# Kernel optimization log

Measured on AMD Instinct MI355X. Metric: run time of the kernel, lower is better.

Reference implementation:

```python
import jax, jax.numpy as jnp
import numpy as np

B, T, C = 2, 2048, 1024
H, D = 16, 64
SCALE = D ** -0.5


def setup_inputs() -> dict:
    key = jax.random.key(0)
    k1, k2, k3 = jax.random.split(key, 3)
    hidden_states = jax.random.normal(k1, (B, T, C), dtype=jnp.float32)
    # rotary tables: standard RoPE angles, shape (T, D//2)
    inv_freq = 1.0 / (10000.0 ** (np.arange(0, D, 2, dtype=np.float32) / D))
    ang = np.arange(T, dtype=np.float32)[:, None] * inv_freq[None, :]
    cos = jnp.asarray(np.cos(ang))
    sin = jnp.asarray(np.sin(ang))
    qkv_w = jax.random.normal(k2, (3 * H * D, C), dtype=jnp.float32) * 0.02
    qkv_b = jnp.zeros((3 * H * D,), dtype=jnp.float32)
    proj_w = jax.random.normal(k3, (C, H * D), dtype=jnp.float32) * 0.02
    proj_b = jnp.zeros((C,), dtype=jnp.float32)
    return dict(hidden_states=hidden_states, cos=cos, sin=sin,
                qkv_w=qkv_w, qkv_b=qkv_b, proj_w=proj_w, proj_b=proj_b)


def _rotary(x, cos, sin):
    # x: (B, H, T, D); cos/sin: (T, D//2) broadcast over batch and heads
    c = cos[None, None, :, :]
    s = sin[None, None, :, :]
    x1, x2 = x[..., ::2], x[..., 1::2]
    return jnp.concatenate([x1 * c - x2 * s, x1 * s + x2 * c], axis=-1)


def reference(hidden_states, cos, sin, qkv_w, qkv_b, proj_w, proj_b):
    b, t, c = hidden_states.shape
    qkv = hidden_states @ qkv_w.T + qkv_b          # (B, T, 3*H*D)
    q, k, v = jnp.split(qkv, 3, axis=-1)
    # (B, T, H, D) -> (B, H, T, D)
    q = q.reshape(b, t, H, D).transpose(0, 2, 1, 3)
    k = k.reshape(b, t, H, D).transpose(0, 2, 1, 3)
    v = v.reshape(b, t, H, D).transpose(0, 2, 1, 3)
    q = _rotary(q, cos, sin)
    k = _rotary(k, cos, sin)
    scores = jnp.einsum('bhqd,bhkd->bhqk', q, k) * SCALE
    # causal mask: -inf above the diagonal
    mask = jnp.triu(jnp.full((t, t), -jnp.inf, dtype=scores.dtype), k=1)
    scores = scores + mask[None, None, :, :]
    attn = jax.nn.softmax(scores, axis=-1)
    out = jnp.einsum('bhqk,bhkd->bhqd', attn, v)   # (B, H, T, D)
    out = out.transpose(0, 2, 1, 3).reshape(b, t, c)
    return out @ proj_w.T + proj_b
```

## Files before the change

### kernel.cpp

```cpp
#include <hip/hip_runtime.h>
#include <stdint.h>

#define B_ 2
#define T_ 2048
#define C_ 1024
#define H_ 16
#define D_ 64
#define SCALE_L2E 0.1803368801111244f

typedef unsigned short ushort_t;
typedef __attribute__((ext_vector_type(8))) __bf16 bf16x8;
typedef __attribute__((ext_vector_type(4))) float f32x4;
typedef __attribute__((ext_vector_type(4))) unsigned short ushort4_t;

__device__ __forceinline__ float bf2f(ushort_t u) {
    union { unsigned int u; float f; } v; v.u = ((unsigned int)u) << 16; return v.f;
}
__device__ __forceinline__ ushort_t f2bf(float f) {
    union { __bf16 h; ushort_t u; } v; v.h = (__bf16)f; return v.u;
}
__device__ __forceinline__ float fexp2(float x) { return __builtin_amdgcn_exp2f(x); }

__device__ __forceinline__ void gl16(const void* g, void* l) {
    __builtin_amdgcn_global_load_lds(
        (const __attribute__((address_space(1))) void*)g,
        (__attribute__((address_space(3))) void*)l, 16, 0, 0);
}

__device__ __forceinline__ f32x4 mfma16(bf16x8 a, bf16x8 b, f32x4 c) {
    return __builtin_amdgcn_mfma_f32_16x16x32_bf16(a, b, c, 0, 0, 0);
}

__global__ __launch_bounds__(256) void cvt3_kernel(const float* __restrict__ a, ushort_t* __restrict__ oa, int na,
                                                   const float* __restrict__ b, ushort_t* __restrict__ ob, int nb,
                                                   const float* __restrict__ c, ushort_t* __restrict__ oc, int nc) {
    int total4 = (na + nb + nc) >> 2;
    int stride = gridDim.x * blockDim.x;
    for (int i = blockIdx.x * blockDim.x + threadIdx.x; i < total4; i += stride) {
        int e = i << 2;
        const float* src; ushort_t* dst; int off;
        if (e < na) { src = a; dst = oa; off = e; }
        else if (e < na + nb) { src = b; dst = ob; off = e - na; }
        else { src = c; dst = oc; off = e - na - nb; }
        float4 v = *(const float4*)(src + off);
        ushort4_t o;
        o.x = f2bf(v.x); o.y = f2bf(v.y); o.z = f2bf(v.z); o.w = f2bf(v.w);
        *(ushort4_t*)(dst + off) = o;
    }
}

__global__ __launch_bounds__(256) void gemm_proj(const ushort_t* __restrict__ A,
                                                 const ushort_t* __restrict__ Bw,
                                                 const float* __restrict__ bias,
                                                 float* __restrict__ outf,
                                                 int M, int N, int K, int nxt) {
    int q = gridDim.x >> 3;
    int nid = (blockIdx.x & 7) * q + (blockIdx.x >> 3);
    int bx = nid % nxt, by = nid / nxt;

    __shared__ ushort_t sm[12288];
    int tid = threadIdx.x, w = tid >> 6, lane = tid & 63;
    int lr = lane >> 4, lc = lane & 15;
    int wr = w >> 1, wc = w & 1;
    int row0 = by * 64, col0 = bx * 128;

    f32x4 acc[2][4];
#pragma unroll
    for (int mf = 0; mf < 2; ++mf)
#pragma unroll
        for (int nf = 0; nf < 4; ++nf) acc[mf][nf] = (f32x4){0.f, 0.f, 0.f, 0.f};

    auto stageg = [&](int buf, int k0) {
        int base = buf * 6144;
        int rA = tid >> 2, cA = (tid & 3) * 8;
        gl16(A + (size_t)(row0 + rA) * K + k0 + cA, &sm[base + tid * 8]);
#pragma unroll
        for (int j = 0; j < 2; ++j) {
            int idx = j * 256 + tid;
            int rB = idx >> 2, cB = (idx & 3) * 8;
            gl16(Bw + (size_t)(col0 + rB) * K + k0 + cB, &sm[base + 2048 + idx * 8]);
        }
    };

    stageg(0, 0);
    asm volatile("s_waitcnt vmcnt(0)" ::: "memory");
    __builtin_amdgcn_s_barrier();

    for (int k0 = 0; k0 < K; k0 += 32) {
        int cur = (k0 >> 5) & 1;
        if (k0 + 32 < K) stageg(cur ^ 1, k0 + 32);
        const ushort_t* As = &sm[cur * 6144];
        const ushort_t* Bs = &sm[cur * 6144 + 2048];
        bf16x8 af[2], bfr[4];
#pragma unroll
        for (int mf = 0; mf < 2; ++mf)
            af[mf] = *(const bf16x8*)&As[(wr * 32 + mf * 16 + lc) * 32 + 8 * lr];
#pragma unroll
        for (int nf = 0; nf < 4; ++nf)
            bfr[nf] = *(const bf16x8*)&Bs[(wc * 64 + nf * 16 + lc) * 32 + 8 * lr];
        __builtin_amdgcn_s_setprio(1);
#pragma unroll
        for (int mf = 0; mf < 2; ++mf)
#pragma unroll
            for (int nf = 0; nf < 4; ++nf)
                acc[mf][nf] = mfma16(af[mf], bfr[nf], acc[mf][nf]);
        __builtin_amdgcn_s_setprio(0);
        asm volatile("s_waitcnt vmcnt(0)" ::: "memory");
        __builtin_amdgcn_s_barrier();
    }
#pragma unroll
    for (int mf = 0; mf < 2; ++mf)
#pragma unroll
        for (int nf = 0; nf < 4; ++nf) {
            int col = col0 + wc * 64 + nf * 16 + lc;
            float bv = bias[col];
#pragma unroll
            for (int r = 0; r < 4; ++r) {
                int row = row0 + wr * 32 + mf * 16 + 4 * lr + r;
                outf[(size_t)row * N + col] = acc[mf][nf][r] + bv;
            }
        }
}

__global__ __launch_bounds__(256) void gemm_qkv_rope(const ushort_t* __restrict__ A,
                                                     const ushort_t* __restrict__ Bw,
                                                     const float* __restrict__ bias,
                                                     const float* __restrict__ cosT,
                                                     const float* __restrict__ sinT,
                                                     ushort_t* __restrict__ Qr,
                                                     ushort_t* __restrict__ Kr,
                                                     ushort_t* __restrict__ Vt) {
    const int K = 1024;
    int nid = (blockIdx.x & 7) * 96 + (blockIdx.x >> 3);
    int bx = nid % 24, by = nid / 24;

    __shared__ ushort_t sm[16384];
    int tid = threadIdx.x, w = tid >> 6, lane = tid & 63;
    int lr = lane >> 4, lc = lane & 15;
    int wr = w >> 1, wc = w & 1;
    int row0 = by * 128, col0 = bx * 128;

    f32x4 acc[4][4];
#pragma unroll
    for (int mf = 0; mf < 4; ++mf)
#pragma unroll
        for (int nf = 0; nf < 4; ++nf) acc[mf][nf] = (f32x4){0.f, 0.f, 0.f, 0.f};

    auto stageg = [&](int buf, int k0) {
#pragma unroll
        for (int j = 0; j < 2; ++j) {
            int idx = j * 256 + tid;
            int r = idx >> 2, c = (idx & 3) * 8;
            gl16(A + (size_t)(row0 + r) * K + k0 + c, &sm[buf * 8192 + idx * 8]);
            gl16(Bw + (size_t)(col0 + r) * K + k0 + c, &sm[buf * 8192 + 4096 + idx * 8]);
        }
    };

    stageg(0, 0);
    asm volatile("s_waitcnt vmcnt(0)" ::: "memory");
    __builtin_amdgcn_s_barrier();

    for (int k0 = 0; k0 < K; k0 += 32) {
        int cur = (k0 >> 5) & 1;
        if (k0 + 32 < K) stageg(cur ^ 1, k0 + 32);
        const ushort_t* As = &sm[cur * 8192];
        const ushort_t* Bs = &sm[cur * 8192 + 4096];
        bf16x8 af[4], bfr[4];
#pragma unroll
        for (int mf = 0; mf < 4; ++mf)
            af[mf] = *(const bf16x8*)&As[(wr * 64 + mf * 16 + lc) * 32 + 8 * lr];
#pragma unroll
        for (int nf = 0; nf < 4; ++nf)
            bfr[nf] = *(const bf16x8*)&Bs[(wc * 64 + nf * 16 + lc) * 32 + 8 * lr];
        __builtin_amdgcn_s_setprio(1);
#pragma unroll
        for (int mf = 0; mf < 4; ++mf)
#pragma unroll
            for (int nf = 0; nf < 4; ++nf)
                acc[mf][nf] = mfma16(af[mf], bfr[nf], acc[mf][nf]);
        __builtin_amdgcn_s_setprio(0);
        asm volatile("s_waitcnt vmcnt(0)" ::: "memory");
        __builtin_amdgcn_s_barrier();
    }

    if (bx < 16) {
        const int typ = bx >> 3;
        ushort_t* dstb = typ ? Kr : Qr;
#pragma unroll
        for (int nf = 0; nf < 4; ++nf) {
            int fullc = col0 + wc * 64 + nf * 16 + lc;
            int gc = fullc & 1023;
            int h = gc >> 6;
            int d2 = (gc & 63) >> 1;
            int odd = gc & 1;
            float bv = bias[fullc];
#pragma unroll
            for (int mf = 0; mf < 4; ++mf)
#pragma unroll
                for (int r = 0; r < 4; ++r) {
                    int row = row0 + wr * 64 + mf * 16 + 4 * lr + r;
                    int bb = row >> 11, t = row & 2047;
                    float v = acc[mf][nf][r] + bv;
                    float pv = __shfl_xor(v, 1, 64);
                    float cth = cosT[t * 32 + d2], sth = sinT[t * 32 + d2];
                    float o = odd ? (pv * sth + v * cth) : (v * cth - pv * sth);
                    if (typ == 0) o *= SCALE_L2E;
                    int od = odd ? (d2 + 32) : d2;
                    dstb[((size_t)(bb * H_ + h) * T_ + t) * D_ + od] = f2bf(o);
                }
        }
    } else {
        int bb = row0 >> 11;
        int tb = row0 & 2047;
#pragma unroll 1
        for (int half = 0; half < 2; ++half) {
            __syncthreads();
            if (wc == half) {
#pragma unroll
                for (int nf = 0; nf < 4; ++nf) {
                    int fullc = col0 + wc * 64 + nf * 16 + lc;
                    float bv = bias[fullc];
                    int c = nf * 16 + lc;
#pragma unroll
                    for (int mf = 0; mf < 4; ++mf)
#pragma unroll
                        for (int r = 0; r < 4; ++r) {
                            int tl = wr * 64 + mf * 16 + 4 * lr + r;
                            sm[c * 136 + tl] = f2bf(acc[mf][nf][r] + bv);
                        }
                }
            }
            __syncthreads();
            int h = ((bx - 16) << 1) + half;
#pragma unroll
            for (int it = 0; it < 8; ++it) {
                int idx = it * 256 + tid;
                int c = idx >> 5, j = idx & 31;
                ushort4_t vv = *(const ushort4_t*)&sm[c * 136 + 4 * j];
                *(ushort4_t*)&Vt[((size_t)(bb * H_ + h) * D_ + c) * T_ + tb + 4 * j] = vv;
            }
        }
    }
}

__global__ __launch_bounds__(256) void attn_kernel(const ushort_t* __restrict__ Qr,
                                                   const ushort_t* __restrict__ Kr,
                                                   const ushort_t* __restrict__ Vt,
                                                   ushort_t* __restrict__ attnb) {
    int id = blockIdx.x;
    int x = id & 7;
    int c = (id >> 3) & 31;
    int g = id >> 8;
    int bh = x + 8 * g;
    int qt;
    if (g == 0) qt = c;
    else if (g == 1) qt = 31 - c;
    else if (g == 2) qt = (c + 16) & 31;
    else qt = 31 - ((c + 16) & 31);
    int b = bh >> 4, h = bh & 15;

    const ushort_t* Qp = Qr + (size_t)bh * T_ * D_;
    const ushort_t* Kp = Kr + (size_t)bh * T_ * D_;
    const ushort_t* Vp = Vt + (size_t)bh * D_ * T_;
    int tid = threadIdx.x, w = tid >> 6, lane = tid & 63;
    int lr = lane >> 4, lc = lane & 15;

    __shared__ ushort_t Ks[2][64 * 64];
    __shared__ ushort_t Vs[2][64 * 64];
    __shared__ ushort_t Ps[4][16 * 64];

    bf16x8 ones;
#pragma unroll
    for (int i = 0; i < 8; ++i) ones[i] = (__bf16)1.0f;

    int srow0 = tid >> 3, sch0 = (tid & 7) ^ (srow0 & 7);
    int srow1 = (256 + tid) >> 3, sch1 = (tid & 7) ^ (srow1 & 7);
    const ushort_t* kg0 = Kp + (size_t)srow0 * D_ + sch0 * 8;
    const ushort_t* kg1 = Kp + (size_t)srow1 * D_ + sch1 * 8;
    const ushort_t* vg0 = Vp + (size_t)srow0 * T_ + sch0 * 8;
    const ushort_t* vg1 = Vp + (size_t)srow1 * T_ + sch1 * 8;
    ushort_t* kl0 = &Ks[0][tid * 8];
    ushort_t* kl1 = &Ks[0][(256 + tid) * 8];
    ushort_t* vl0 = &Vs[0][tid * 8];
    ushort_t* vl1 = &Vs[0][(256 + tid) * 8];

    auto stage = [&](int buf, int kt) {
        size_t koff = (size_t)kt * 64 * D_;
        size_t voff = (size_t)kt * 64;
        size_t lb = (size_t)buf * 4096;
        gl16(kg0 + koff, kl0 + lb);
        gl16(vg0 + voff, vl0 + lb);
        gl16(kg1 + koff, kl1 + lb);
        gl16(vg1 + voff, vl1 + lb);
    };

    int qrow = qt * 64 + w * 16 + lc;
    bf16x8 qf0 = *(const bf16x8*)(Qp + (size_t)qrow * D_ + 8 * lr);
    bf16x8 qf1 = *(const bf16x8*)(Qp + (size_t)qrow * D_ + 32 + 8 * lr);

    float m_s = 0.f;
    f32x4 acc[4], acc_l;
#pragma unroll
    for (int f = 0; f < 4; ++f) acc[f] = (f32x4){0.f, 0.f, 0.f, 0.f};
    acc_l = (f32x4){0.f, 0.f, 0.f, 0.f};

    stage(0, 0);
    asm volatile("s_waitcnt vmcnt(0)" ::: "memory");
    __builtin_amdgcn_s_barrier();

    for (int kt = 0; kt <= qt; ++kt) {
        int cur = kt & 1;
        if (kt < qt) stage(cur ^ 1, kt + 1);
        int t0 = kt * 64;

        f32x4 sv[4];
        __builtin_amdgcn_s_setprio(1);
#pragma unroll
        for (int f = 0; f < 4; ++f) {
            sv[f] = (f32x4){-m_s, -m_s, -m_s, -m_s};
            int row = 16 * f + lc;
#pragma unroll
            for (int kk = 0; kk < 2; ++kk) {
                bf16x8 kf = *(const bf16x8*)&Ks[cur][row * 64 + (((lr + 4 * kk) ^ (row & 7)) * 8)];
                sv[f] = mfma16(kf, kk ? qf1 : qf0, sv[f]);
            }
        }
        __builtin_amdgcn_s_setprio(0);

        float lm = -1e30f;
        if (kt == qt) {
#pragma unroll
            for (int f = 0; f < 4; ++f)
#pragma unroll
                for (int r = 0; r < 4; ++r) {
                    int kg = t0 + 16 * f + 4 * lr + r;
                    float v = sv[f][r];
                    v = (kg > qrow) ? -1e30f : v;
                    sv[f][r] = v;
                    lm = fmaxf(lm, v);
                }
        } else {
#pragma unroll
            for (int f = 0; f < 4; ++f)
#pragma unroll
                for (int r = 0; r < 4; ++r)
                    lm = fmaxf(lm, sv[f][r]);
        }

        if (!__all(lm <= 8.0f)) {
            float tm = fmaxf(lm, __shfl_xor(lm, 16, 64));
            tm = fmaxf(tm, __shfl_xor(tm, 32, 64));
            float d = fmaxf(tm, 0.f);
            m_s += d;
            float alpha = fexp2(-d);
            float ar[4];
#pragma unroll
            for (int r = 0; r < 4; ++r) ar[r] = __shfl(alpha, 4 * lr + r, 64);
#pragma unroll
            for (int r = 0; r < 4; ++r) {
                acc_l[r] *= ar[r];
#pragma unroll
                for (int f = 0; f < 4; ++f) acc[f][r] *= ar[r];
            }
#pragma unroll
            for (int f = 0; f < 4; ++f)
#pragma unroll
                for (int r = 0; r < 4; ++r) sv[f][r] -= d;
        }

#pragma unroll
        for (int f = 0; f < 4; ++f) {
            ushort4_t pk;
            pk.x = f2bf(fexp2(sv[f][0]));
            pk.y = f2bf(fexp2(sv[f][1]));
            pk.z = f2bf(fexp2(sv[f][2]));
            pk.w = f2bf(fexp2(sv[f][3]));
            *(ushort4_t*)&Ps[w][lc * 64 + (((4 * f + lr) ^ (lc & 14)) << 2)] = pk;
        }

        __builtin_amdgcn_s_setprio(1);
#pragma unroll
        for (int kk = 0; kk < 2; ++kk) {
            bf16x8 pf = *(const bf16x8*)&Ps[w][lc * 64 + (((8 * kk + 2 * lr) ^ (lc & 14)) << 2)];
            acc_l = mfma16(pf, ones, acc_l);
#pragma unroll
            for (int f = 0; f < 4; ++f) {
                int vrow = 16 * f + lc;
                bf16x8 vfr = *(const bf16x8*)&Vs[cur][vrow * 64 + (((lr + 4 * kk) ^ (vrow & 7)) * 8)];
                acc[f] = mfma16(pf, vfr, acc[f]);
            }
        }
        __builtin_amdgcn_s_setprio(0);

        asm volatile("s_waitcnt vmcnt(0)" ::: "memory");
        __builtin_amdgcn_s_barrier();
    }

    float inv[4];
#pragma unroll
    for (int r = 0; r < 4; ++r) inv[r] = __builtin_amdgcn_rcpf(acc_l[r]);
#pragma unroll
    for (int f = 0; f < 4; ++f)
#pragma unroll
        for (int r = 0; r < 4; ++r) {
            int t = qt * 64 + w * 16 + 4 * lr + r;
            attnb[((size_t)(b * T_ + t)) * 1024 + h * 64 + 16 * f + lc] =
                f2bf(acc[f][r] * inv[r]);
        }
}

extern "C" void kernel_launch(void* const* d_in, const int* in_sizes, int n_in,
                              void* d_out, int out_size, void* d_ws, size_t ws_size,
                              hipStream_t stream) {
    const float* hs     = (const float*)d_in[0];
    const float* cosp   = (const float*)d_in[1];
    const float* sinp   = (const float*)d_in[2];
    const float* qkv_w  = (const float*)d_in[3];
    const float* qkv_b  = (const float*)d_in[4];
    const float* proj_w = (const float*)d_in[5];
    const float* proj_b = (const float*)d_in[6];
    float* out = (float*)d_out;

    const int M = B_ * T_;
    ushort_t* Xb     = (ushort_t*)d_ws;
    ushort_t* Wqkvb  = Xb + (size_t)M * C_;
    ushort_t* Wprojb = Wqkvb + (size_t)3072 * C_;
    ushort_t* Qr     = Wprojb + (size_t)C_ * C_;
    ushort_t* Kr     = Qr + (size_t)B_ * H_ * T_ * D_;
    ushort_t* Vt     = Kr + (size_t)B_ * H_ * T_ * D_;
    ushort_t* attnb  = Vt + (size_t)B_ * H_ * T_ * D_;

    cvt3_kernel<<<2048, 256, 0, stream>>>(hs, Xb, M * C_,
                                          qkv_w, Wqkvb, 3072 * C_,
                                          proj_w, Wprojb, C_ * C_);

    gemm_qkv_rope<<<768, 256, 0, stream>>>(Xb, Wqkvb, qkv_b, cosp, sinp, Qr, Kr, Vt);

    attn_kernel<<<1024, 256, 0, stream>>>(Qr, Kr, Vt, attnb);

    gemm_proj<<<512, 256, 0, stream>>>(attnb, Wprojb, proj_b, out, M, C_, C_, 8);
}
```

Before: 117.1 us.

## Triple-buffer global-to-LDS loads in GEMMs and attention with partial vmcnt waits

The QKV GEMM, projection GEMM and flash-attention kernels move from double to triple buffering of their LDS tiles. Each loop prefetches two stages ahead and waits only for the older stage's loads via a partial vmcnt count. This is meant to hide global load latency better behind the MFMA work. The cost is 50% more LDS per block, which may reduce occupancy, and the vmcnt counts must exactly match the number of loads each thread issues per stage.

```diff
diff --git a/kernel.cpp b/kernel.cpp
--- a/kernel.cpp
+++ b/kernel.cpp
@@ -58,7 +58,7 @@
     int nid = (blockIdx.x & 7) * q + (blockIdx.x >> 3);
     int bx = nid % nxt, by = nid / nxt;
 
-    __shared__ ushort_t sm[12288];
+    __shared__ ushort_t sm[18432];
     int tid = threadIdx.x, w = tid >> 6, lane = tid & 63;
     int lr = lane >> 4, lc = lane & 15;
     int wr = w >> 1, wc = w & 1;
@@ -83,12 +83,15 @@
     };
 
     stageg(0, 0);
-    asm volatile("s_waitcnt vmcnt(0)" ::: "memory");
+    stageg(1, 32);
+    asm volatile("s_waitcnt vmcnt(3)" ::: "memory");
     __builtin_amdgcn_s_barrier();
 
     for (int k0 = 0; k0 < K; k0 += 32) {
-        int cur = (k0 >> 5) & 1;
-        if (k0 + 32 < K) stageg(cur ^ 1, k0 + 32);
+        int ks = k0 >> 5;
+        int cur = ks % 3;
+        bool st = (k0 + 64 < K);
+        if (st) stageg((ks + 2) % 3, k0 + 64);
         const ushort_t* As = &sm[cur * 6144];
         const ushort_t* Bs = &sm[cur * 6144 + 2048];
         bf16x8 af[2], bfr[4];
@@ -105,7 +108,11 @@
             for (int nf = 0; nf < 4; ++nf)
                 acc[mf][nf] = mfma16(af[mf], bfr[nf], acc[mf][nf]);
         __builtin_amdgcn_s_setprio(0);
-        asm volatile("s_waitcnt vmcnt(0)" ::: "memory");
+        if (st) {
+            asm volatile("s_waitcnt vmcnt(3)" ::: "memory");
+        } else {
+            asm volatile("s_waitcnt vmcnt(0)" ::: "memory");
+        }
         __builtin_amdgcn_s_barrier();
     }
 #pragma unroll
@@ -134,7 +141,7 @@
     int nid = (blockIdx.x & 7) * 96 + (blockIdx.x >> 3);
     int bx = nid % 24, by = nid / 24;
 
-    __shared__ ushort_t sm[16384];
+    __shared__ ushort_t sm[24576];
     int tid = threadIdx.x, w = tid >> 6, lane = tid & 63;
     int lr = lane >> 4, lc = lane & 15;
     int wr = w >> 1, wc = w & 1;
@@ -157,12 +164,15 @@
     };
 
     stageg(0, 0);
-    asm volatile("s_waitcnt vmcnt(0)" ::: "memory");
+    stageg(1, 32);
+    asm volatile("s_waitcnt vmcnt(4)" ::: "memory");
     __builtin_amdgcn_s_barrier();
 
     for (int k0 = 0; k0 < K; k0 += 32) {
-        int cur = (k0 >> 5) & 1;
-        if (k0 + 32 < K) stageg(cur ^ 1, k0 + 32);
+        int ks = k0 >> 5;
+        int cur = ks % 3;
+        bool st = (k0 + 64 < K);
+        if (st) stageg((ks + 2) % 3, k0 + 64);
         const ushort_t* As = &sm[cur * 8192];
         const ushort_t* Bs = &sm[cur * 8192 + 4096];
         bf16x8 af[4], bfr[4];
@@ -179,7 +189,11 @@
             for (int nf = 0; nf < 4; ++nf)
                 acc[mf][nf] = mfma16(af[mf], bfr[nf], acc[mf][nf]);
         __builtin_amdgcn_s_setprio(0);
-        asm volatile("s_waitcnt vmcnt(0)" ::: "memory");
+        if (st) {
+            asm volatile("s_waitcnt vmcnt(4)" ::: "memory");
+        } else {
+            asm volatile("s_waitcnt vmcnt(0)" ::: "memory");
+        }
         __builtin_amdgcn_s_barrier();
     }
 
@@ -265,8 +279,8 @@
     int tid = threadIdx.x, w = tid >> 6, lane = tid & 63;
     int lr = lane >> 4, lc = lane & 15;
 
-    __shared__ ushort_t Ks[2][64 * 64];
-    __shared__ ushort_t Vs[2][64 * 64];
+    __shared__ ushort_t Ks[3][64 * 64];
+    __shared__ ushort_t Vs[3][64 * 64];
     __shared__ ushort_t Ps[4][16 * 64];
 
     bf16x8 ones;
@@ -305,12 +319,18 @@
     acc_l = (f32x4){0.f, 0.f, 0.f, 0.f};
 
     stage(0, 0);
-    asm volatile("s_waitcnt vmcnt(0)" ::: "memory");
+    if (qt >= 1) {
+        stage(1, 1);
+        asm volatile("s_waitcnt vmcnt(4)" ::: "memory");
+    } else {
+        asm volatile("s_waitcnt vmcnt(0)" ::: "memory");
+    }
     __builtin_amdgcn_s_barrier();
 
     for (int kt = 0; kt <= qt; ++kt) {
-        int cur = kt & 1;
-        if (kt < qt) stage(cur ^ 1, kt + 1);
+        int cur = kt % 3;
+        bool st = (kt + 2 <= qt);
+        if (st) stage((kt + 2) % 3, kt + 2);
         int t0 = kt * 64;
 
         f32x4 sv[4];
@@ -392,7 +412,11 @@
         }
         __builtin_amdgcn_s_setprio(0);
 
-        asm volatile("s_waitcnt vmcnt(0)" ::: "memory");
+        if (st) {
+            asm volatile("s_waitcnt vmcnt(4)" ::: "memory");
+        } else {
+            asm volatile("s_waitcnt vmcnt(0)" ::: "memory");
+        }
         __builtin_amdgcn_s_barrier();
     }
 
```

After: 130.5 us. 11.4% more time.
